# Performance work log

Hardware: AMD Instinct MI355X
Metric: run time of the kernel (lower is better)

The kernel has to match this reference:

```python
import jax, jax.numpy as jnp
import numpy as np

B, A, C = 16, 16384, 81
TOP_K = 50
CONF_THRESH = 0.5
IOU_THRESH = 0.5
VAR0, VAR1 = 0.1, 0.2          # cfg['variance']
IMG_HW = 1.0                   # cfg['min_dim']/img_size = 320/320
MIN_SIZE = 0.0
NEG = -jnp.inf


def setup_inputs() -> dict:
    key = jax.random.key(0)
    k1, k2, k3 = jax.random.split(key, 3)
    conf_preds = jax.random.uniform(k1, (B, A, C), dtype=jnp.float32)
    loc_delta = jax.random.normal(k2, (B, A, 4), dtype=jnp.float32)
    anchors = jax.random.uniform(k3, (A, 4), dtype=jnp.float32)  # cxcywh priors in [0,1)
    return {"conf_preds": conf_preds, "loc_delta": loc_delta, "anchors": anchors}


def _decode_clip(loc, anchors):
    # SSD decode: cxcy = prior_cxcy + loc_xy*v0*prior_wh ; wh = prior_wh*exp(loc_wh*v1)
    cxcy = anchors[..., :2] + loc[..., :2] * VAR0 * anchors[..., 2:]
    wh = anchors[..., 2:] * jnp.exp(loc[..., 2:] * VAR1)
    x1y1 = cxcy - wh * 0.5
    x2y2 = x1y1 + wh
    boxes = jnp.concatenate([x1y1, x2y2], axis=-1)  # [..., 4] xyxy
    return jnp.clip(boxes, 0.0, IMG_HW)            # clip_boxes_to_image((1,1))


def _nms_single(boxes, s):
    # boxes: [A,4] xyxy, s: [A] scores with invalid entries already at -inf.
    # Greedy NMS, fixed TOP_K iterations (torchvision semantics: suppress iou > thresh).
    areas = (boxes[:, 2] - boxes[:, 0]) * (boxes[:, 3] - boxes[:, 1])

    def step(s, _):
        i = jnp.argmax(s)
        take = s[i] > NEG
        b = boxes[i]
        xx1 = jnp.maximum(b[0], boxes[:, 0])
        yy1 = jnp.maximum(b[1], boxes[:, 1])
        xx2 = jnp.minimum(b[2], boxes[:, 2])
        yy2 = jnp.minimum(b[3], boxes[:, 3])
        inter = jnp.maximum(xx2 - xx1, 0.0) * jnp.maximum(yy2 - yy1, 0.0)
        iou = inter / (areas[i] + areas - inter)
        s = jnp.where(take & (iou > IOU_THRESH), NEG, s)
        s = s.at[i].set(NEG)  # guarantee progress
        return s, (i, take)

    _, (idx, take) = jax.lax.scan(step, s, None, length=TOP_K)
    return idx, take  # [TOP_K] int, [TOP_K] bool


def reference(conf_preds, loc_delta, anchors):
    boxes = _decode_clip(loc_delta, anchors)                # [B,A,4]
    conf = jnp.transpose(conf_preds, (0, 2, 1))             # [B,C,A]
    # remove_small_boxes(min_size=0) as a mask (all-true here, kept for fidelity)
    w = boxes[..., 2] - boxes[..., 0]
    h = boxes[..., 3] - boxes[..., 1]
    valid = (w >= MIN_SIZE) & (h >= MIN_SIZE)               # [B,A]
    masked = jnp.where((conf > CONF_THRESH) & valid[:, None, :], conf, NEG)  # [B,C,A]

    sg = jax.lax.stop_gradient
    nms_c = jax.vmap(_nms_single, in_axes=(None, 0))        # over classes
    nms_bc = jax.vmap(nms_c, in_axes=(0, 0))                # over batch
    idx, take = nms_bc(sg(boxes), sg(masked))               # [B,C,K]

    scores_sel = jnp.take_along_axis(conf, idx, axis=2)     # [B,C,K]
    b_idx = jnp.arange(boxes.shape[0])[:, None, None]
    boxes_sel = boxes[b_idx, idx]                           # [B,C,K,4]
    preds = jnp.concatenate([
        jnp.where(take, scores_sel, 0.0)[..., None],
        jnp.where(take[..., None], boxes_sel, 0.0),
    ], axis=-1)                                             # [B,C,K,5]
    return preds
```

## Files before the change

### kernel.cpp

```cpp
#include <hip/hip_runtime.h>
#include <math.h>

#define NB 16
#define NA 16384
#define NC 81
#define TOPK 50
#define NBK 255
#define TRC 8960
#define NEGF (-__builtin_inff())
#define SUPC 0.5000000298023223876953125

typedef unsigned long long ull;

#define WS_CONFT_OFF  ((size_t)4194304)
#define WS_FULL  (WS_CONFT_OFF + (size_t)NB * NC * NA)

__global__ __launch_bounds__(256) void decode_k(const float* __restrict__ loc,
                                                const float* __restrict__ anc,
                                                float* __restrict__ boxes) {
#pragma clang fp contract(off)
    int i = blockIdx.x * 256 + threadIdx.x;
    if (i >= NB * NA) return;
    int a = i & (NA - 1);
    float4 an = ((const float4*)anc)[a];
    float4 ld = ((const float4*)loc)[i];
    float cx = an.x + (ld.x * 0.1f) * an.z;
    float cy = an.y + (ld.y * 0.1f) * an.w;
    float w = an.z * (float)exp((double)(ld.z * 0.2f));
    float h = an.w * (float)exp((double)(ld.w * 0.2f));
    float x1 = cx - w * 0.5f;
    float y1 = cy - h * 0.5f;
    float x2 = x1 + w;
    float y2 = y1 + h;
    x1 = fminf(fmaxf(x1, 0.f), 1.f);
    y1 = fminf(fmaxf(y1, 0.f), 1.f);
    x2 = fminf(fmaxf(x2, 0.f), 1.f);
    y2 = fminf(fmaxf(y2, 0.f), 1.f);
    ((float4*)boxes)[i] = make_float4(x1, y1, x2, y2);
}

__device__ __forceinline__ unsigned enc8(float v) {
    unsigned e = 0xFFu;
    if (v > 0.5f) {
        unsigned d = 255u - ((__float_as_uint(v) >> 15) & 0xFFu);
        e = (d > 254u) ? 254u : d;
    }
    return e;
}

#define TSLAB 512
__global__ __launch_bounds__(256) void transq_k(const float* __restrict__ conf,
                                                unsigned char* __restrict__ confT) {
    __shared__ unsigned char code[TSLAB * NC];
    const int b = blockIdx.y;
    const int slab = blockIdx.x;
    const float4* src = (const float4*)(conf + ((size_t)b * NA + (size_t)slab * TSLAB) * NC);
    const int t = threadIdx.x;
    for (int i = t; i < (TSLAB * NC) / 4; i += 256) {
        float4 v = src[i];
        unsigned wrd = enc8(v.x) | (enc8(v.y) << 8) | (enc8(v.z) << 16) | (enc8(v.w) << 24);
        *(unsigned*)&code[4 * i] = wrd;
    }
    __syncthreads();
    const int lane = t & 63, wv = t >> 6;
    for (int c = wv; c < NC; c += 4) {
        ull v = 0ull;
#pragma unroll
        for (int j = 0; j < 8; ++j)
            v |= (ull)code[(8 * lane + j) * NC + c] << (8 * j);
        *(ull*)(confT + ((size_t)b * NC + c) * NA + (size_t)slab * TSLAB + 8 * lane) = v;
    }
}

__global__ __launch_bounds__(256, 6) void nmsB5_k(const unsigned char* __restrict__ confT,
                                                  const float* __restrict__ conf,
                                                  const float* __restrict__ boxes,
                                                  float* __restrict__ out) {
#pragma clang fp contract(off)
    const int blk = blockIdx.x;
    const int b = blk / NC, c = blk - b * NC;
    const int t = threadIdx.x;
    const int lane = t & 63, wv = t >> 6;

    __shared__ unsigned short s_ix[TRC];
    __shared__ unsigned s_off[NBK + 1];
    __shared__ unsigned s_aux[NBK];
    __shared__ float s_acc[TOPK][5];
    __shared__ float4 s_cbox[256];
    __shared__ unsigned long long s_kill[4];
    __shared__ int s_ctrl[16];

    const uint4* row16 = (const uint4*)(confT + ((size_t)b * NC + c) * NA);
    const float* cp = conf + ((size_t)b * NA) * NC + c;
    const float4* bb = (const float4*)boxes + (size_t)b * NA;
    float* orow = out + ((size_t)b * NC + c) * (TOPK * 5);

    if (t < NBK) s_aux[t] = 0u;
    if (t == 0) { s_ctrl[0] = 0; s_ctrl[8] = 0; s_ctrl[12] = 0; }
    __syncthreads();
#pragma unroll
    for (int r = 0; r < 4; ++r) {
        uint4 q = row16[t + 256 * r];
        unsigned wrds[4] = {q.x, q.y, q.z, q.w};
#pragma unroll
        for (int m = 0; m < 4; ++m)
#pragma unroll
            for (int k = 0; k < 4; ++k) {
                unsigned bk = (wrds[m] >> (8 * k)) & 0xFFu;
                if (bk != 0xFFu) atomicAdd(&s_aux[bk], 1u);
            }
    }
    __syncthreads();
    if (t < NBK) atomicMax(&s_ctrl[8], (int)s_aux[t]);
    if (t == 0) s_off[0] = 0u;
    if (t < NBK) s_off[t + 1] = s_aux[t];
    __syncthreads();
    for (int d = 1; d < 256; d <<= 1) {
        unsigned v0 = 0u;
        if (t < NBK) v0 = (1 + t - d >= 1) ? s_off[1 + t - d] : 0u;
        __syncthreads();
        if (t < NBK) s_off[1 + t] += v0;
        __syncthreads();
    }

    if (s_ctrl[8] <= TRC) {
        while (true) {
            if (t == 0) {
                int lo = s_ctrl[12];
                int hi = lo;
                while (hi < NBK && s_off[hi + 1] - s_off[lo] <= (unsigned)TRC) hi++;
                s_ctrl[13] = hi;
            }
            __syncthreads();
            const int trLo = s_ctrl[12], trHi = s_ctrl[13];
            const unsigned tbase = s_off[trLo], tend = s_off[trHi];
            if (tbase == tend) break;
            for (int i = trLo + t; i < trHi; i += 256) s_aux[i] = s_off[i] - tbase;
            __syncthreads();
#pragma unroll
            for (int r = 0; r < 4; ++r) {
                uint4 q = row16[t + 256 * r];
                unsigned wrds[4] = {q.x, q.y, q.z, q.w};
                int base_a = 16 * (t + 256 * r);
#pragma unroll
                for (int m = 0; m < 4; ++m)
#pragma unroll
                    for (int k = 0; k < 4; ++k) {
                        int bk = (int)((wrds[m] >> (8 * k)) & 0xFFu);
                        if (bk >= trLo && bk < trHi)
                            s_ix[atomicAdd(&s_aux[bk], 1u)] =
                                (unsigned short)(base_a + 4 * m + k);
                    }
            }
            if (t == 0) s_ctrl[7] = trLo;
            __syncthreads();

            while (true) {
                if (t == 0) {
                    int bp = s_ctrl[7];
                    int mode;
                    if (bp >= trHi || s_off[bp] >= tend) {
                        mode = 2;
                    } else {
                        unsigned pos = s_off[bp] - tbase;
                        int bpl = bp;
                        unsigned q = pos;
                        for (int w = 0; w < 4; ++w) {
                            s_ctrl[2 + w] = (int)q;
                            while (bpl < trHi && (s_off[bpl + 1] - tbase - q) <= 64u) bpl++;
                            q = (bpl < trHi) ? s_off[bpl] - tbase : tend - tbase;
                        }
                        s_ctrl[6] = (int)q;
                        s_ctrl[7] = bpl;
                        mode = 0;
                        if (q == pos) {
                            mode = 1;
                            s_ctrl[9] = (int)pos;
                            s_ctrl[10] = (int)(s_off[bp + 1] - tbase);
                            s_ctrl[7] = bp + 1;
                        }
                    }
                    s_ctrl[11] = mode;
                }
                __syncthreads();
                const int mode = s_ctrl[11];
                if (mode == 2) break;
                const int nacc0 = s_ctrl[0];

                if (mode == 0) {
                    const unsigned q0 = (unsigned)s_ctrl[2 + wv];
                    const unsigned q1 = (unsigned)s_ctrl[3 + wv];
                    const int mw = (int)(q1 - q0);
                    const bool valid = lane < mw;
                    int ii = (int)q0 + lane; if (ii > TRC - 1) ii = TRC - 1;
                    int a = valid ? (int)s_ix[ii] : 0;
                    float4 bxv = bb[a];
                    if (!valid) bxv = make_float4(0.f, 0.f, 0.f, 0.f);
                    s_cbox[wv * 64 + lane] = bxv;
                    float mar = (bxv.z - bxv.x) * (bxv.w - bxv.y);
                    bool kill = !valid;
                    for (int j = 0; j < nacc0; ++j) {
                        float xx1 = fmaxf(s_acc[j][0], bxv.x), yy1 = fmaxf(s_acc[j][1], bxv.y);
                        float xx2 = fminf(s_acc[j][2], bxv.z), yy2 = fminf(s_acc[j][3], bxv.w);
                        float iw = fmaxf(xx2 - xx1, 0.f), ih = fmaxf(yy2 - yy1, 0.f);
                        float inter = iw * ih;
                        float den = (s_acc[j][4] + mar) - inter;
                        if ((double)inter > (double)den * SUPC) kill = true;
                    }
                    unsigned long long km = __ballot(kill);
                    if (lane == 0) s_kill[wv] = km;
                    __syncthreads();

                    if (wv == 0) {
                        int na = nacc0;
                        for (int cc = 0; cc < 4 && na < TOPK; ++cc) {
                            const unsigned e0 = (unsigned)s_ctrl[2 + cc];
                            const unsigned e1 = (unsigned)s_ctrl[3 + cc];
                            const int mc = (int)(e1 - e0);
                            if (mc <= 0) continue;
                            unsigned long long alive = ~s_kill[cc];
                            if (mc < 64) alive &= (1ull << mc) - 1ull;
                            int jj = (int)e0 + lane; if (jj > TRC - 1) jj = TRC - 1;
                            int aj = (lane < mc) ? (int)s_ix[jj] : 0;
                            float myscore = cp[(size_t)aj * NC];
                            float4 mybx = s_cbox[cc * 64 + lane];
                            float mar2 = (mybx.z - mybx.x) * (mybx.w - mybx.y);
                            for (int j = nacc0; j < na && alive; ++j) {
                                float xx1 = fmaxf(s_acc[j][0], mybx.x), yy1 = fmaxf(s_acc[j][1], mybx.y);
                                float xx2 = fminf(s_acc[j][2], mybx.z), yy2 = fminf(s_acc[j][3], mybx.w);
                                float iw = fmaxf(xx2 - xx1, 0.f), ih = fmaxf(yy2 - yy1, 0.f);
                                float inter = iw * ih;
                                float den = (s_acc[j][4] + mar2) - inter;
                                bool sup = ((double)inter > (double)den * SUPC);
                                alive &= ~__ballot(sup);
                            }
                            unsigned long long mykey =
                                ((unsigned long long)__float_as_uint(myscore) << 32) |
                                (unsigned)(16383 - aj);
                            while (alive && na < TOPK) {
                                unsigned long long kk = ((alive >> lane) & 1ull) ? mykey : 0ull;
                                int src = lane;
                                for (int off = 32; off; off >>= 1) {
                                    unsigned long long ok = __shfl_xor(kk, off);
                                    int osrc = __shfl_xor(src, off);
                                    if (ok > kk) { kk = ok; src = osrc; }
                                }
                                float4 wb = s_cbox[cc * 64 + src];
                                float wscore = __shfl(myscore, src);
                                float war = (wb.z - wb.x) * (wb.w - wb.y);
                                if (lane == 0) {
                                    orow[na * 5 + 0] = wscore;
                                    orow[na * 5 + 1] = wb.x; orow[na * 5 + 2] = wb.y;
                                    orow[na * 5 + 3] = wb.z; orow[na * 5 + 4] = wb.w;
                                    s_acc[na][0] = wb.x; s_acc[na][1] = wb.y;
                                    s_acc[na][2] = wb.z; s_acc[na][3] = wb.w;
                                    s_acc[na][4] = war;
                                }
                                na++;
                                alive &= ~(1ull << src);
                                if (alive) {
                                    float xx1 = fmaxf(wb.x, mybx.x), yy1 = fmaxf(wb.y, mybx.y);
                                    float xx2 = fminf(wb.z, mybx.z), yy2 = fminf(wb.w, mybx.w);
                                    float iw = fmaxf(xx2 - xx1, 0.f), ih = fmaxf(yy2 - yy1, 0.f);
                                    float inter = iw * ih;
                                    float den = (war + mar2) - inter;
                                    bool sup = ((double)inter > (double)den * SUPC);
                                    alive &= ~__ballot(sup);
                                }
                            }
                        }
                        if (lane == 0) s_ctrl[0] = na;
                    }
                    __syncthreads();
                } else {
                    const int e0 = s_ctrl[9], e1 = s_ctrl[10];
                    if (wv == 0) {
                        int na = s_ctrl[0];
                        while (na < TOPK) {
                            unsigned long long bk = 0ull; int bpos = 0;
                            for (int i = e0 + lane; i < e1; i += 64) {
                                int av = (int)s_ix[i];
                                if (av != 0xFFFF) {
                                    float v = cp[(size_t)av * NC];
                                    unsigned long long k =
                                        ((unsigned long long)__float_as_uint(v) << 32) |
                                        (unsigned)(16383 - av);
                                    if (k > bk) { bk = k; bpos = i; }
                                }
                            }
                            for (int off = 32; off; off >>= 1) {
                                unsigned long long ok = __shfl_xor(bk, off);
                                int op = __shfl_xor(bpos, off);
                                if (ok > bk) { bk = ok; bpos = op; }
                            }
                            if (bk == 0ull) break;
                            int a = (int)s_ix[bpos];
                            float wscore = __uint_as_float((unsigned)(bk >> 32));
                            if (lane == 0) s_ix[bpos] = 0xFFFFu;
                            float4 wb = bb[a];
                            float war = (wb.z - wb.x) * (wb.w - wb.y);
                            bool sup = false;
                            if (lane < na) {
                                float xx1 = fmaxf(s_acc[lane][0], wb.x), yy1 = fmaxf(s_acc[lane][1], wb.y);
                                float xx2 = fminf(s_acc[lane][2], wb.z), yy2 = fminf(s_acc[lane][3], wb.w);
                                float iw = fmaxf(xx2 - xx1, 0.f), ih = fmaxf(yy2 - yy1, 0.f);
                                float inter = iw * ih;
                                float den = (s_acc[lane][4] + war) - inter;
                                sup = ((double)inter > (double)den * SUPC);
                            }
                            if (__ballot(sup) == 0ull) {
                                if (lane == 0) {
                                    orow[na * 5 + 0] = wscore;
                                    orow[na * 5 + 1] = wb.x; orow[na * 5 + 2] = wb.y;
                                    orow[na * 5 + 3] = wb.z; orow[na * 5 + 4] = wb.w;
                                    s_acc[na][0] = wb.x; s_acc[na][1] = wb.y;
                                    s_acc[na][2] = wb.z; s_acc[na][3] = wb.w;
                                    s_acc[na][4] = war;
                                }
                                na++;
                            }
                        }
                        if (lane == 0) s_ctrl[0] = na;
                    }
                    __syncthreads();
                }
                if (s_ctrl[0] >= TOPK) break;
            }
            if (s_ctrl[0] >= TOPK || trHi >= NBK) break;
            if (t == 0) s_ctrl[12] = trHi;
            __syncthreads();
        }
    } else {
        float hi = 1.0f, delta = 0.02f;
        while (true) {
            if (s_ctrl[0] >= TOPK || hi <= 0.5f) break;
            float lo = fmaxf(hi - delta, 0.5f);
            if (t == 0) s_ctrl[1] = 0;
            __syncthreads();
            for (int a = t; a < NA; a += 256) {
                float v = cp[(size_t)a * NC];
                if (v > lo && v <= hi) {
                    int p = atomicAdd(&s_ctrl[1], 1);
                    if (p < TRC) s_ix[p] = (unsigned short)a;
                }
            }
            __syncthreads();
            int m = s_ctrl[1];
            if (m > TRC) { delta *= 0.5f; continue; }
            if (wv == 0) {
                int na = s_ctrl[0];
                while (na < TOPK) {
                    unsigned long long bk = 0ull; int bpos = 0;
                    for (int i = lane; i < m; i += 64) {
                        int av = (int)s_ix[i];
                        if (av != 0xFFFF) {
                            float v = cp[(size_t)av * NC];
                            unsigned long long k =
                                ((unsigned long long)__float_as_uint(v) << 32) |
                                (unsigned)(16383 - av);
                            if (k > bk) { bk = k; bpos = i; }
                        }
                    }
                    for (int off = 32; off; off >>= 1) {
                        unsigned long long ok = __shfl_xor(bk, off);
                        int op = __shfl_xor(bpos, off);
                        if (ok > bk) { bk = ok; bpos = op; }
                    }
                    if (bk == 0ull) break;
                    int a = (int)s_ix[bpos];
                    float wscore = __uint_as_float((unsigned)(bk >> 32));
                    if (lane == 0) s_ix[bpos] = 0xFFFFu;
                    float4 wb = bb[a];
                    float war = (wb.z - wb.x) * (wb.w - wb.y);
                    bool sup = false;
                    if (lane < na) {
                        float xx1 = fmaxf(s_acc[lane][0], wb.x), yy1 = fmaxf(s_acc[lane][1], wb.y);
                        float xx2 = fminf(s_acc[lane][2], wb.z), yy2 = fminf(s_acc[lane][3], wb.w);
                        float iw = fmaxf(xx2 - xx1, 0.f), ih = fmaxf(yy2 - yy1, 0.f);
                        float inter = iw * ih;
                        float den = (s_acc[lane][4] + war) - inter;
                        sup = ((double)inter > (double)den * SUPC);
                    }
                    if (__ballot(sup) == 0ull) {
                        if (lane == 0) {
                            orow[na * 5 + 0] = wscore;
                            orow[na * 5 + 1] = wb.x; orow[na * 5 + 2] = wb.y;
                            orow[na * 5 + 3] = wb.z; orow[na * 5 + 4] = wb.w;
                            s_acc[na][0] = wb.x; s_acc[na][1] = wb.y;
                            s_acc[na][2] = wb.z; s_acc[na][3] = wb.w;
                            s_acc[na][4] = war;
                        }
                        na++;
                    }
                }
                if (lane == 0) s_ctrl[0] = na;
            }
            __syncthreads();
            hi = lo;
        }
    }

    __syncthreads();
    const int naF = s_ctrl[0];
    for (int z = naF * 5 + t; z < TOPK * 5; z += 256) orow[z] = 0.f;
}

#define OTHREADS 1024
#define OCAP 10240
#define OJMAX 10

__global__ __launch_bounds__(OTHREADS) void nms_old_k(const float* __restrict__ conf,
                                                      const float* __restrict__ boxes,
                                                      float* __restrict__ out) {
#pragma clang fp contract(off)
    const int blk = blockIdx.x;
    const int b = blk / NC, c = blk - b * NC;
    const int t = threadIdx.x;
    const int lane = t & 63, wid = t >> 6;
    __shared__ float s_val[OCAP];
    __shared__ unsigned short s_idx[OCAP];
    __shared__ float s_ps[2][16];
    __shared__ int s_pa[2][16];
    __shared__ int s_n;
    if (t == 0) s_n = 0;
    __syncthreads();
    const float* cp = conf + ((size_t)b * NA) * NC + c;
    float v[NA / OTHREADS];
#pragma unroll
    for (int r = 0; r < NA / OTHREADS; ++r)
        v[r] = cp[(size_t)(r * OTHREADS + t) * NC];
#pragma unroll
    for (int r = 0; r < NA / OTHREADS; ++r) {
        int a = r * OTHREADS + t;
        bool alive = v[r] > 0.5f;
        unsigned long long m = __ballot(alive);
        int cnt = __popcll(m);
        int base = 0;
        if (lane == 0 && cnt) base = atomicAdd(&s_n, cnt);
        base = __shfl(base, 0);
        if (alive) {
            int p = base + __popcll(m & ((1ull << lane) - 1));
            if (p < OCAP) { s_val[p] = v[r]; s_idx[p] = (unsigned short)a; }
        }
    }
    __syncthreads();
    int n = s_n; if (n > OCAP) n = OCAP;
    const int jn = (n + OTHREADS - 1) / OTHREADS;
    const float4* bb = (const float4*)boxes + (size_t)b * NA;
    float sc[OJMAX]; float4 bx[OJMAX]; int ia[OJMAX];
#pragma unroll
    for (int j = 0; j < OJMAX; ++j) {
        sc[j] = NEGF; ia[j] = 0x7fffffff; bx[j] = make_float4(0.f, 0.f, 0.f, 0.f);
        int p = j * OTHREADS + t;
        if (p < n) { sc[j] = s_val[p]; ia[j] = (int)s_idx[p]; bx[j] = bb[ia[j]]; }
    }
    float* orow = out + (size_t)blk * (TOPK * 5);
    int k = 0;
    for (; k < TOPK; ++k) {
        float ms = NEGF; int ma = 0x7fffffff;
#pragma unroll
        for (int j = 0; j < OJMAX; ++j) {
            if (j < jn) {
                bool better = (sc[j] > ms) || (sc[j] == ms && ia[j] < ma);
                ms = better ? sc[j] : ms;
                ma = better ? ia[j] : ma;
            }
        }
#pragma unroll
        for (int off = 32; off; off >>= 1) {
            float os = __shfl_xor(ms, off);
            int oa = __shfl_xor(ma, off);
            if (os > ms || (os == ms && oa < ma)) { ms = os; ma = oa; }
        }
        int pb = k & 1;
        if (lane == 0) { s_ps[pb][wid] = ms; s_pa[pb][wid] = ma; }
        __syncthreads();
        float wsv = NEGF; int wa = 0x7fffffff;
#pragma unroll
        for (int w = 0; w < 16; ++w) {
            float os = s_ps[pb][w]; int oa = s_pa[pb][w];
            if (os > wsv || (os == wsv && oa < wa)) { wsv = os; wa = oa; }
        }
        if (!(wsv > NEGF)) break;
        float4 wb = bb[wa];
        float warea = (wb.z - wb.x) * (wb.w - wb.y);
        if (t == 0) {
            orow[k * 5 + 0] = wsv;
            orow[k * 5 + 1] = wb.x; orow[k * 5 + 2] = wb.y;
            orow[k * 5 + 3] = wb.z; orow[k * 5 + 4] = wb.w;
        }
#pragma unroll
        for (int j = 0; j < OJMAX; ++j) {
            if (j < jn) {
                float xx1 = fmaxf(wb.x, bx[j].x);
                float yy1 = fmaxf(wb.y, bx[j].y);
                float xx2 = fminf(wb.z, bx[j].z);
                float yy2 = fminf(wb.w, bx[j].w);
                float iw = fmaxf(xx2 - xx1, 0.f);
                float ih = fmaxf(yy2 - yy1, 0.f);
                float inter = iw * ih;
                float aj = (bx[j].z - bx[j].x) * (bx[j].w - bx[j].y);
                float denom = (warea + aj) - inter;
                bool supp = ((double)inter > (double)denom * SUPC) || (ia[j] == wa);
                if (supp) sc[j] = NEGF;
            }
        }
    }
    for (int z = k * 5 + t; z < TOPK * 5; z += OTHREADS) orow[z] = 0.f;
}

extern "C" void kernel_launch(void* const* d_in, const int* in_sizes, int n_in,
                              void* d_out, int out_size, void* d_ws, size_t ws_size,
                              hipStream_t stream) {
    const float* conf = (const float*)d_in[0];
    const float* loc  = (const float*)d_in[1];
    const float* anc  = (const float*)d_in[2];
    float* boxes = (float*)d_ws;

    decode_k<<<(NB * NA + 255) / 256, 256, 0, stream>>>(loc, anc, boxes);

    if (ws_size >= WS_FULL) {
        unsigned char* confT = (unsigned char*)((char*)d_ws + WS_CONFT_OFF);
        dim3 tg(NA / TSLAB, NB);
        transq_k<<<tg, 256, 0, stream>>>(conf, confT);
        nmsB5_k<<<NB * NC, 256, 0, stream>>>(confT, conf, boxes, (float*)d_out);
    } else {
        nms_old_k<<<NB * NC, OTHREADS, 0, stream>>>(conf, boxes, (float*)d_out);
    }
}
```

Baseline: 210.6 us.

## Fuse decode into transpose kernel, halve slab size, use float IoU test

Merges the box decode kernel into the conf transpose/quantize kernel via a z-dimension split, removing one launch. The transpose slab shrinks from 512 to 256 anchors and writes 4-byte words instead of 8-byte ones. Accepted boxes are stored as float4 plus a separate area array to get vectorized LDS reads. The double-precision IoU>0.5 comparison is replaced by an FMA-based float test meant to be equivalent, which drops the slow fp64 ops but risks edge-case rounding differences.

```diff
diff --git a/kernel.cpp b/kernel.cpp
--- a/kernel.cpp
+++ b/kernel.cpp
@@ -15,12 +15,23 @@
 #define WS_CONFT_OFF  ((size_t)4194304)
 #define WS_FULL  (WS_CONFT_OFF + (size_t)NB * NC * NA)
 
-__global__ __launch_bounds__(256) void decode_k(const float* __restrict__ loc,
-                                                const float* __restrict__ anc,
-                                                float* __restrict__ boxes) {
+__device__ __forceinline__ bool iou_gt_half(float inter, float den) {
+    return fmaf(den, -0.5f, inter) > den * 0x1p-25f;
+}
+
+__device__ __forceinline__ unsigned enc8(float v) {
+    unsigned e = 0xFFu;
+    if (v > 0.5f) {
+        unsigned d = 255u - ((__float_as_uint(v) >> 15) & 0xFFu);
+        e = (d > 254u) ? 254u : d;
+    }
+    return e;
+}
+
+__device__ __forceinline__ void decode_body(int i, const float* __restrict__ loc,
+                                            const float* __restrict__ anc,
+                                            float* __restrict__ boxes) {
 #pragma clang fp contract(off)
-    int i = blockIdx.x * 256 + threadIdx.x;
-    if (i >= NB * NA) return;
     int a = i & (NA - 1);
     float4 an = ((const float4*)anc)[a];
     float4 ld = ((const float4*)loc)[i];
@@ -39,23 +50,28 @@
     ((float4*)boxes)[i] = make_float4(x1, y1, x2, y2);
 }
 
-__device__ __forceinline__ unsigned enc8(float v) {
-    unsigned e = 0xFFu;
-    if (v > 0.5f) {
-        unsigned d = 255u - ((__float_as_uint(v) >> 15) & 0xFFu);
-        e = (d > 254u) ? 254u : d;
-    }
-    return e;
-}
-
-#define TSLAB 512
-__global__ __launch_bounds__(256) void transq_k(const float* __restrict__ conf,
-                                                unsigned char* __restrict__ confT) {
+__global__ __launch_bounds__(256) void decode_k(const float* __restrict__ loc,
+                                                const float* __restrict__ anc,
+                                                float* __restrict__ boxes) {
+    int i = blockIdx.x * 256 + threadIdx.x;
+    if (i < NB * NA) decode_body(i, loc, anc, boxes);
+}
+
+#define TSLAB 256
+__global__ __launch_bounds__(256) void prep_k(const float* __restrict__ conf,
+                                              const float* __restrict__ loc,
+                                              const float* __restrict__ anc,
+                                              float* __restrict__ boxes,
+                                              unsigned char* __restrict__ confT) {
     __shared__ unsigned char code[TSLAB * NC];
-    const int b = blockIdx.y;
-    const int slab = blockIdx.x;
+    const int t = threadIdx.x;
+    if (blockIdx.z == 1) {
+        int i = (blockIdx.x + 64 * blockIdx.y) * 256 + t;
+        if (i < NB * NA) decode_body(i, loc, anc, boxes);
+        return;
+    }
+    const int b = blockIdx.y, slab = blockIdx.x;
     const float4* src = (const float4*)(conf + ((size_t)b * NA + (size_t)slab * TSLAB) * NC);
-    const int t = threadIdx.x;
     for (int i = t; i < (TSLAB * NC) / 4; i += 256) {
         float4 v = src[i];
         unsigned wrd = enc8(v.x) | (enc8(v.y) << 8) | (enc8(v.z) << 16) | (enc8(v.w) << 24);
@@ -64,15 +80,15 @@
     __syncthreads();
     const int lane = t & 63, wv = t >> 6;
     for (int c = wv; c < NC; c += 4) {
-        ull v = 0ull;
-#pragma unroll
-        for (int j = 0; j < 8; ++j)
-            v |= (ull)code[(8 * lane + j) * NC + c] << (8 * j);
-        *(ull*)(confT + ((size_t)b * NC + c) * NA + (size_t)slab * TSLAB + 8 * lane) = v;
-    }
-}
-
-__global__ __launch_bounds__(256, 6) void nmsB5_k(const unsigned char* __restrict__ confT,
+        unsigned v = 0u;
+#pragma unroll
+        for (int j = 0; j < 4; ++j)
+            v |= (unsigned)code[(4 * lane + j) * NC + c] << (8 * j);
+        *(unsigned*)(confT + ((size_t)b * NC + c) * NA + (size_t)slab * TSLAB + 4 * lane) = v;
+    }
+}
+
+__global__ __launch_bounds__(256, 6) void nmsB6_k(const unsigned char* __restrict__ confT,
                                                   const float* __restrict__ conf,
                                                   const float* __restrict__ boxes,
                                                   float* __restrict__ out) {
@@ -85,7 +101,8 @@
     __shared__ unsigned short s_ix[TRC];
     __shared__ unsigned s_off[NBK + 1];
     __shared__ unsigned s_aux[NBK];
-    __shared__ float s_acc[TOPK][5];
+    __shared__ float4 s_abox[TOPK];
+    __shared__ float s_aarea[TOPK];
     __shared__ float4 s_cbox[256];
     __shared__ unsigned long long s_kill[4];
     __shared__ int s_ctrl[16];
@@ -200,12 +217,14 @@
                     float mar = (bxv.z - bxv.x) * (bxv.w - bxv.y);
                     bool kill = !valid;
                     for (int j = 0; j < nacc0; ++j) {
-                        float xx1 = fmaxf(s_acc[j][0], bxv.x), yy1 = fmaxf(s_acc[j][1], bxv.y);
-                        float xx2 = fminf(s_acc[j][2], bxv.z), yy2 = fminf(s_acc[j][3], bxv.w);
+                        float4 ab = s_abox[j];
+                        float aa = s_aarea[j];
+                        float xx1 = fmaxf(ab.x, bxv.x), yy1 = fmaxf(ab.y, bxv.y);
+                        float xx2 = fminf(ab.z, bxv.z), yy2 = fminf(ab.w, bxv.w);
                         float iw = fmaxf(xx2 - xx1, 0.f), ih = fmaxf(yy2 - yy1, 0.f);
                         float inter = iw * ih;
-                        float den = (s_acc[j][4] + mar) - inter;
-                        if ((double)inter > (double)den * SUPC) kill = true;
+                        float den = (aa + mar) - inter;
+                        if (iou_gt_half(inter, den)) kill = true;
                     }
                     unsigned long long km = __ballot(kill);
                     if (lane == 0) s_kill[wv] = km;
@@ -226,12 +245,14 @@
                             float4 mybx = s_cbox[cc * 64 + lane];
                             float mar2 = (mybx.z - mybx.x) * (mybx.w - mybx.y);
                             for (int j = nacc0; j < na && alive; ++j) {
-                                float xx1 = fmaxf(s_acc[j][0], mybx.x), yy1 = fmaxf(s_acc[j][1], mybx.y);
-                                float xx2 = fminf(s_acc[j][2], mybx.z), yy2 = fminf(s_acc[j][3], mybx.w);
+                                float4 ab = s_abox[j];
+                                float aa = s_aarea[j];
+                                float xx1 = fmaxf(ab.x, mybx.x), yy1 = fmaxf(ab.y, mybx.y);
+                                float xx2 = fminf(ab.z, mybx.z), yy2 = fminf(ab.w, mybx.w);
                                 float iw = fmaxf(xx2 - xx1, 0.f), ih = fmaxf(yy2 - yy1, 0.f);
                                 float inter = iw * ih;
-                                float den = (s_acc[j][4] + mar2) - inter;
-                                bool sup = ((double)inter > (double)den * SUPC);
+                                float den = (aa + mar2) - inter;
+                                bool sup = iou_gt_half(inter, den);
                                 alive &= ~__ballot(sup);
                             }
                             unsigned long long mykey =
@@ -252,9 +273,8 @@
                                     orow[na * 5 + 0] = wscore;
                                     orow[na * 5 + 1] = wb.x; orow[na * 5 + 2] = wb.y;
                                     orow[na * 5 + 3] = wb.z; orow[na * 5 + 4] = wb.w;
-                                    s_acc[na][0] = wb.x; s_acc[na][1] = wb.y;
-                                    s_acc[na][2] = wb.z; s_acc[na][3] = wb.w;
-                                    s_acc[na][4] = war;
+                                    s_abox[na] = wb;
+                                    s_aarea[na] = war;
                                 }
                                 na++;
                                 alive &= ~(1ull << src);
@@ -264,7 +284,7 @@
                                     float iw = fmaxf(xx2 - xx1, 0.f), ih = fmaxf(yy2 - yy1, 0.f);
                                     float inter = iw * ih;
                                     float den = (war + mar2) - inter;
-                                    bool sup = ((double)inter > (double)den * SUPC);
+                                    bool sup = iou_gt_half(inter, den);
                                     alive &= ~__ballot(sup);
                                 }
                             }
@@ -301,21 +321,22 @@
                             float war = (wb.z - wb.x) * (wb.w - wb.y);
                             bool sup = false;
                             if (lane < na) {
-                                float xx1 = fmaxf(s_acc[lane][0], wb.x), yy1 = fmaxf(s_acc[lane][1], wb.y);
-                                float xx2 = fminf(s_acc[lane][2], wb.z), yy2 = fminf(s_acc[lane][3], wb.w);
+                                float4 ab = s_abox[lane];
+                                float aa = s_aarea[lane];
+                                float xx1 = fmaxf(ab.x, wb.x), yy1 = fmaxf(ab.y, wb.y);
+                                float xx2 = fminf(ab.z, wb.z), yy2 = fminf(ab.w, wb.w);
                                 float iw = fmaxf(xx2 - xx1, 0.f), ih = fmaxf(yy2 - yy1, 0.f);
                                 float inter = iw * ih;
-                                float den = (s_acc[lane][4] + war) - inter;
-                                sup = ((double)inter > (double)den * SUPC);
+                                float den = (aa + war) - inter;
+                                sup = iou_gt_half(inter, den);
                             }
                             if (__ballot(sup) == 0ull) {
                                 if (lane == 0) {
                                     orow[na * 5 + 0] = wscore;
                                     orow[na * 5 + 1] = wb.x; orow[na * 5 + 2] = wb.y;
                                     orow[na * 5 + 3] = wb.z; orow[na * 5 + 4] = wb.w;
-                                    s_acc[na][0] = wb.x; s_acc[na][1] = wb.y;
-                                    s_acc[na][2] = wb.z; s_acc[na][3] = wb.w;
-                                    s_acc[na][4] = war;
+                                    s_abox[na] = wb;
+                                    s_aarea[na] = war;
                                 }
                                 na++;
                             }
@@ -374,21 +395,22 @@
                     float war = (wb.z - wb.x) * (wb.w - wb.y);
                     bool sup = false;
                     if (lane < na) {
-                        float xx1 = fmaxf(s_acc[lane][0], wb.x), yy1 = fmaxf(s_acc[lane][1], wb.y);
-                        float xx2 = fminf(s_acc[lane][2], wb.z), yy2 = fminf(s_acc[lane][3], wb.w);
+                        float4 ab = s_abox[lane];
+                        float aa = s_aarea[lane];
+                        float xx1 = fmaxf(ab.x, wb.x), yy1 = fmaxf(ab.y, wb.y);
+                        float xx2 = fminf(ab.z, wb.z), yy2 = fminf(ab.w, wb.w);
                         float iw = fmaxf(xx2 - xx1, 0.f), ih = fmaxf(yy2 - yy1, 0.f);
                         float inter = iw * ih;
-                        float den = (s_acc[lane][4] + war) - inter;
-                        sup = ((double)inter > (double)den * SUPC);
+                        float den = (aa + war) - inter;
+                        sup = iou_gt_half(inter, den);
                     }
                     if (__ballot(sup) == 0ull) {
                         if (lane == 0) {
                             orow[na * 5 + 0] = wscore;
                             orow[na * 5 + 1] = wb.x; orow[na * 5 + 2] = wb.y;
                             orow[na * 5 + 3] = wb.z; orow[na * 5 + 4] = wb.w;
-                            s_acc[na][0] = wb.x; s_acc[na][1] = wb.y;
-                            s_acc[na][2] = wb.z; s_acc[na][3] = wb.w;
-                            s_acc[na][4] = war;
+                            s_abox[na] = wb;
+                            s_aarea[na] = war;
                         }
                         na++;
                     }
@@ -517,14 +539,13 @@
     const float* anc  = (const float*)d_in[2];
     float* boxes = (float*)d_ws;
 
-    decode_k<<<(NB * NA + 255) / 256, 256, 0, stream>>>(loc, anc, boxes);
-
     if (ws_size >= WS_FULL) {
         unsigned char* confT = (unsigned char*)((char*)d_ws + WS_CONFT_OFF);
-        dim3 tg(NA / TSLAB, NB);
-        transq_k<<<tg, 256, 0, stream>>>(conf, confT);
-        nmsB5_k<<<NB * NC, 256, 0, stream>>>(confT, conf, boxes, (float*)d_out);
+        dim3 tg(NA / TSLAB, NB, 2);
+        prep_k<<<tg, 256, 0, stream>>>(conf, loc, anc, boxes, confT);
+        nmsB6_k<<<NB * NC, 256, 0, stream>>>(confT, conf, boxes, (float*)d_out);
     } else {
+        decode_k<<<(NB * NA + 255) / 256, 256, 0, stream>>>(loc, anc, boxes);
         nms_old_k<<<NB * NC, OTHREADS, 0, stream>>>(conf, boxes, (float*)d_out);
     }
 }
```

After: 207.6 us. Within noise of the previous version (-1.4%).
